# Optimization experiments

Measured on AMD Instinct MI355X. Metric: run time of the kernel, lower is better.

Reference implementation:

```python
import jax, jax.numpy as jnp
import numpy as np

# Bit-slice quantization config (MSB-first; first 1-bit slice is the sign slice)
INPUT_SLICE = (1, 2, 2, 2)    # 7 bits total
WEIGHT_SLICE = (1, 2, 2, 2)   # 7 bits total
INPUT_GRAN = 32               # input quant granularity along K (per unfolded row)
WEIGHT_GRAN_K = 32            # weight quant granularity along K
WEIGHT_GRAN_N = 32            # weight quant granularity along N
STRIDE = 1
PAD = 1
KSIZE = 3


def _quantize(x, max_abs, total_bits):
    """Symmetric per-granule quantization to signed total_bits integers."""
    max_val = float((1 << (total_bits - 1)) - 1)
    scale = max_abs / max_val
    scale = jnp.where(scale == 0, jnp.ones_like(scale), scale)
    q = jnp.clip(jnp.round(x / scale), -max_val, max_val)
    return q, scale


def _slice_recombine(q, slice_bits):
    """Emulate the bit-slice path: decompose signed int q (two's complement)
    into slices per slice_bits (MSB first), then recombine exactly as the
    crossbar MapReduce accumulation 'sum_i slice_i * 2^offset_i' would."""
    t = int(sum(slice_bits))
    qi = q.astype(jnp.int32)
    u = jnp.where(qi < 0, qi + (1 << t), qi)  # two's complement unsigned rep
    recomb = jnp.zeros_like(u)
    off = t
    for b in slice_bits:  # fixed, small slice loop
        off -= b
        s = (u >> off) & ((1 << b) - 1)
        recomb = recomb + (s << off)
    recomb = jnp.where(recomb >= (1 << (t - 1)), recomb - (1 << t), recomb)
    return recomb.astype(jnp.float32)


def _fake_quant_input(x):
    # x: (B, L, K) unfolded activations; granularity (1, INPUT_GRAN)
    B, L, K = x.shape
    g = INPUT_GRAN
    xg = x.reshape(B, L, K // g, g)
    max_abs = jnp.max(jnp.abs(xg), axis=-1, keepdims=True)
    q, scale = _quantize(xg, max_abs, sum(INPUT_SLICE))
    q = _slice_recombine(q, INPUT_SLICE)
    deq = (q * scale).reshape(B, L, K)
    # straight-through estimator (matches custom autograd conv2d_mem_func)
    return x + jax.lax.stop_gradient(deq - x)


def _fake_quant_weight(w):
    # w: (K, N) reshaped weight; granularity (WEIGHT_GRAN_K, WEIGHT_GRAN_N)
    K, N = w.shape
    gk, gn = WEIGHT_GRAN_K, WEIGHT_GRAN_N
    wg = w.reshape(K // gk, gk, N // gn, gn)
    max_abs = jnp.max(jnp.abs(wg), axis=(1, 3), keepdims=True)
    q, scale = _quantize(wg, max_abs, sum(WEIGHT_SLICE))
    q = _slice_recombine(q, WEIGHT_SLICE)
    deq = (q * scale).reshape(K, N)
    return w + jax.lax.stop_gradient(deq - w)


def _unfold(x, k, stride, pad):
    # torch.F.unfold semantics -> (B, L, C*k*k), C-major ordering
    B, C, H, W = x.shape
    xp = jnp.pad(x, ((0, 0), (0, 0), (pad, pad), (pad, pad)))
    Ho = (H + 2 * pad - k) // stride + 1
    Wo = (W + 2 * pad - k) // stride + 1
    cols = []
    for ki in range(k):  # fixed small kernel loop
        for kj in range(k):
            cols.append(xp[:, :, ki:ki + stride * Ho:stride, kj:kj + stride * Wo:stride])
    patches = jnp.stack(cols, axis=2)              # (B, C, k*k, Ho, Wo)
    patches = patches.reshape(B, C * k * k, Ho * Wo)
    return patches.transpose(0, 2, 1), Ho, Wo      # (B, L, K)


def setup_inputs() -> dict:
    key = jax.random.key(0)
    k1, k2, k3 = jax.random.split(key, 3)
    B, C, H, W = 8, 256, 56, 56
    N = 256
    fan_in = C * KSIZE * KSIZE
    x = jax.random.normal(k1, (B, C, H, W), dtype=jnp.float32)
    weight = jax.random.normal(k2, (N, C, KSIZE, KSIZE), dtype=jnp.float32) / np.sqrt(fan_in)
    bias = jax.random.normal(k3, (N,), dtype=jnp.float32) / np.sqrt(fan_in)
    return {"input": x, "weight": weight, "bias": bias}


def reference(input, weight, bias):
    B = input.shape[0]
    N = weight.shape[0]
    cols, Ho, Wo = _unfold(input, KSIZE, STRIDE, PAD)     # (B, L, K)
    w2d = weight.reshape(N, -1).T                         # (K, N)
    xq = _fake_quant_input(cols)
    wq = _fake_quant_weight(w2d)
    out = jnp.einsum('blk,kn->bln', xq, wq) + bias        # (B, L, N)
    out = out.transpose(0, 2, 1).reshape(B, N, Ho, Wo)    # fold with 1x1 kernel
    return out
```

## Files before the change

### kernel.cpp

```cpp
#include <hip/hip_runtime.h>
#include <hip/hip_bf16.h>
#include <stdint.h>

#define KD 2304
#define LD 3136
#define ND 256
#define MD 25088
#define CD 256
#define PITCH 64
#define PROWS 58
#define PLANE (PROWS * PITCH)

typedef __bf16 bf16x8 __attribute__((ext_vector_type(8)));
typedef float f32x4 __attribute__((ext_vector_type(4)));
typedef float f32x4u __attribute__((ext_vector_type(4), aligned(4)));

__device__ __forceinline__ void gload_lds16(const void* g, void* l) {
  __builtin_amdgcn_global_load_lds(
      (const __attribute__((address_space(1))) unsigned int*)g,
      (__attribute__((address_space(3))) unsigned int*)l, 16, 0, 0);
}

__global__ __launch_bounds__(256) void pad_kernel(
    const float* __restrict__ x, float* __restrict__ xpad) {
  const int plane = blockIdx.x;
  const float* src = x + (size_t)plane * LD;
  float* dst = xpad + (size_t)plane * PLANE;
  const int cc4 = (threadIdx.x & 15) * 4;
  const int r0 = threadIdx.x >> 4;
#pragma unroll
  for (int p = 0; p < 4; ++p) {
    const int r = r0 + p * 16;
    if (r >= PROWS) continue;
    f32x4 o = {0.f, 0.f, 0.f, 0.f};
    if (r >= 1 && r <= 56) {
      const float* srow = src + (r - 1) * 56;
      if (cc4 == 0) {
        f32x4u v = *(const f32x4u*)(srow);
        o[1] = v[0]; o[2] = v[1]; o[3] = v[2];
      } else if (cc4 <= 52) {
        o = *(const f32x4u*)(srow + cc4 - 1);
      } else if (cc4 == 56) {
        f32x4u v = *(const f32x4u*)(srow + 52);
        o[0] = v[3];
      }
    }
    *(f32x4*)(dst + r * PITCH + cc4) = o;
  }
}

__global__ __launch_bounds__(256) void quant_w_kernel(
    const float* __restrict__ w, __hip_bfloat16* __restrict__ wqT) {
  const int gk = blockIdx.x % 72;
  const int gn = blockIdx.x / 72;
  const int n = gn * 32 + (threadIdx.x >> 3);
  const int k = gk * 32 + (threadIdx.x & 7) * 4;
  const float4 v = *(const float4*)(w + (size_t)n * KD + k);
  float a = fmaxf(fmaxf(fabsf(v.x), fabsf(v.y)), fmaxf(fabsf(v.z), fabsf(v.w)));
#pragma unroll
  for (int m = 1; m <= 32; m <<= 1) a = fmaxf(a, __shfl_xor(a, m, 64));
  __shared__ float red[4];
  if ((threadIdx.x & 63) == 0) red[threadIdx.x >> 6] = a;
  __syncthreads();
  const float mx = fmaxf(fmaxf(red[0], red[1]), fmaxf(red[2], red[3]));
  const float r63 = (mx == 0.f) ? 0.f : 63.f / mx;
  const float scale = mx * (1.f / 63.f);
  ushort4 o;
  o.x = __builtin_bit_cast(unsigned short, __float2bfloat16(rintf(v.x * r63) * scale));
  o.y = __builtin_bit_cast(unsigned short, __float2bfloat16(rintf(v.y * r63) * scale));
  o.z = __builtin_bit_cast(unsigned short, __float2bfloat16(rintf(v.z * r63) * scale));
  o.w = __builtin_bit_cast(unsigned short, __float2bfloat16(rintf(v.w * r63) * scale));
  *(ushort4*)((unsigned short*)wqT + (size_t)n * KD + k) = o;
}

template <int KP0>
__device__ __forceinline__ void qload(const float* __restrict__ pb, int p0, int c0,
                                      f32x4u (&win)[5][3]) {
  constexpr int NCH = (KP0 + 31) / 9 + 1;
#pragma unroll
  for (int dc = 0; dc < 5; ++dc) {
    if (dc >= NCH) continue;
    const int tlo = (dc == 0) ? KP0 : 0;
    const int thi = (dc == NCH - 1) ? (KP0 + 31 - 9 * (NCH - 1)) : 8;
#pragma unroll
    for (int di = 0; di < 3; ++di) {
      if (di >= tlo / 3 && di <= thi / 3)
        win[dc][di] = *(const f32x4u*)(pb + p0 + (c0 + dc) * PLANE + di * PITCH);
    }
  }
}

template <int KP0>
__device__ __forceinline__ void qfinish(const f32x4u (&win)[5][3],
                                        char* as_row, unsigned cbase, unsigned swz) {
  float v[32];
#pragma unroll
  for (int t = 0; t < 32; ++t) {
    const int idx = KP0 + t;
    v[t] = win[idx / 9][(idx % 9) / 3][(idx % 9) % 3];
  }
  float m16[16];
#pragma unroll
  for (int t = 0; t < 16; ++t)
    m16[t] = fmaxf(__builtin_fabsf(v[2 * t]), __builtin_fabsf(v[2 * t + 1]));
#pragma unroll
  for (int t = 0; t < 8; ++t) m16[t] = fmaxf(m16[t], m16[t + 8]);
#pragma unroll
  for (int t = 0; t < 4; ++t) m16[t] = fmaxf(m16[t], m16[t + 4]);
  const float mx = fmaxf(fmaxf(m16[0], m16[1]), fmaxf(m16[2], m16[3]));
  float r63 = 63.f * __builtin_amdgcn_rcpf(mx);
  r63 = (mx == 0.f) ? 0.f : r63;
  const float scale = mx * (1.f / 63.f);
  unsigned pk[16];
#pragma unroll
  for (int t = 0; t < 16; ++t) {
    const float a = rintf(v[2 * t] * r63) * scale;
    const float b = rintf(v[2 * t + 1] * r63) * scale;
    unsigned d;
    asm("v_cvt_pk_bf16_f32 %0, %1, %2" : "=v"(d) : "v"(a), "v"(b));
    pk[t] = d;
  }
#pragma unroll
  for (int s = 0; s < 4; ++s) {
    uint4 o = {pk[4 * s], pk[4 * s + 1], pk[4 * s + 2], pk[4 * s + 3]};
    *(uint4*)(as_row + ((cbase + (unsigned)(s * 16)) ^ swz)) = o;
  }
}

__device__ __forceinline__ void stage_ns(const unsigned short* __restrict__ wsrc,
                                         int k0, int lane, int w, char* Ns) {
#pragma unroll
  for (int sg = 0; sg < 16; ++sg) {
    const int c = w * 16 + sg;
    const int rowN = c * 4 + (lane >> 4);
    const int u = (lane & 15) ^ (rowN & 7);
    gload_lds16(wsrc + (size_t)rowN * KD + k0 + u * 8,
                Ns + c * 1024 + lane * 16);
  }
}

__device__ __forceinline__ void mfma_phase(const char* As, const char* Ns,
                                           f32x4 (&acc)[4][4], int w, int lq, int hv) {
  const unsigned swq = (unsigned)((lq & 7) << 4);
#pragma unroll
  for (int kk = 0; kk < 4; ++kk) {
    const unsigned ko = (unsigned)(kk * 64 + hv * 16);
    bf16x8 af[4], bfr[4];
#pragma unroll
    for (int ifr = 0; ifr < 4; ++ifr) {
      const unsigned rn = (unsigned)(w * 64 + ifr * 16 + lq);
      af[ifr] = *(const bf16x8*)(Ns + rn * 256u + (ko ^ swq));
    }
#pragma unroll
    for (int jfr = 0; jfr < 4; ++jfr) {
      const unsigned rm = (unsigned)(jfr * 16 + lq);
      bfr[jfr] = *(const bf16x8*)(As + rm * 256u + (ko ^ swq));
    }
#pragma unroll
    for (int ifr = 0; ifr < 4; ++ifr)
#pragma unroll
      for (int jfr = 0; jfr < 4; ++jfr)
        acc[ifr][jfr] = __builtin_amdgcn_mfma_f32_16x16x32_bf16(
            af[ifr], bfr[jfr], acc[ifr][jfr], 0, 0, 0);
  }
}

#define PH(RR, W) ((128 * (RR) + 32 * (W)) % 9)

__global__ __launch_bounds__(256, 2) void fused_gemm_kernel(
    const float* __restrict__ xpad, const __hip_bfloat16* __restrict__ wqT,
    const float* __restrict__ bias, float* __restrict__ out) {
  extern __shared__ char smem[];
  char* As = smem;
  char* Ns = smem + 16384;
  const int tid = threadIdx.x;
  const int lane = tid & 63;
  const int w = __builtin_amdgcn_readfirstlane(tid >> 6);

  const int bid = blockIdx.x;
  const int mt = (bid & 7) * 49 + (bid >> 3);
  const int m0 = mt * 64;

  const int b = m0 / LD;
  const int l = m0 - b * LD + lane;
  const int i = l / 56;
  const int j = l - i * 56;
  const float* pb = xpad + (size_t)b * CD * PLANE;
  const int p0 = i * PITCH + j;
  char* as_row = As + lane * 256;
  const unsigned swz = (unsigned)((lane & 7) << 4);
  const unsigned short* wqTu = (const unsigned short*)wqT;

  const int lq = lane & 15, hv = lane >> 4;

  f32x4 acc[4][4] = {};
  f32x4u win[5][3];

#define QLOADX(RS, Rg)                                                        \
  {                                                                           \
    const int c0_ = (128 * (Rg) + 32 * w) / 9;                                \
    switch (w) {                                                              \
      case 0:  qload<PH(RS, 0)>(pb, p0, c0_, win); break;                     \
      case 1:  qload<PH(RS, 1)>(pb, p0, c0_, win); break;                     \
      case 2:  qload<PH(RS, 2)>(pb, p0, c0_, win); break;                     \
      default: qload<PH(RS, 3)>(pb, p0, c0_, win); break;                     \
    }                                                                         \
  }

#define QFINX(RS)                                                             \
  switch (w) {                                                                \
    case 0:  qfinish<PH(RS, 0)>(win, as_row, 0u,   swz); break;               \
    case 1:  qfinish<PH(RS, 1)>(win, as_row, 64u,  swz); break;               \
    case 2:  qfinish<PH(RS, 2)>(win, as_row, 128u, swz); break;               \
    default: qfinish<PH(RS, 3)>(win, as_row, 192u, swz); break;               \
  }

#define STEP(r)                                                               \
  {                                                                           \
    const int Rg = ss9 + (r);                                                 \
    stage_ns(wqTu, Rg * 128, lane, w, Ns);          \
    QFINX(r);                                          \
    if ((r) < 8 || ss == 0) { QLOADX((r) + 1, Rg + 1); }   \
    __syncthreads();                                                          \
    mfma_phase(As, Ns, acc, w, lq, hv);                                       \
    __syncthreads();                                                          \
  }

  QLOADX(0, 0);

  for (int ss = 0; ss < 2; ++ss) {
    const int ss9 = ss * 9;
    STEP(0) STEP(1) STEP(2) STEP(3) STEP(4) STEP(5) STEP(6) STEP(7) STEP(8)
  }
#undef STEP
#undef QFINX
#undef QLOADX

#pragma unroll
  for (int ifr = 0; ifr < 4; ++ifr) {
    const int nb = w * 64 + ifr * 16 + hv * 4;
    const float4 b4 = *(const float4*)&bias[nb];
#pragma unroll
    for (int jfr = 0; jfr < 4; ++jfr) {
      const int m = m0 + jfr * 16 + lq;
      const int ll = m - b * LD;
      float* op = out + ((size_t)b * ND + nb) * LD + ll;
      op[0]      = acc[ifr][jfr].x + b4.x;
      op[LD]     = acc[ifr][jfr].y + b4.y;
      op[2 * LD] = acc[ifr][jfr].z + b4.z;
      op[3 * LD] = acc[ifr][jfr].w + b4.w;
    }
  }
}

extern "C" void kernel_launch(void* const* d_in, const int* in_sizes, int n_in,
                              void* d_out, int out_size, void* d_ws, size_t ws_size,
                              hipStream_t stream) {
  const float* x = (const float*)d_in[0];
  const float* wgt = (const float*)d_in[1];
  const float* bias = (const float*)d_in[2];
  float* out = (float*)d_out;

  float* xpad = (float*)d_ws;
  __hip_bfloat16* wqT = (__hip_bfloat16*)((char*)d_ws + 30408704);

  pad_kernel<<<8 * CD, 256, 0, stream>>>(x, xpad);
  quant_w_kernel<<<576, 256, 0, stream>>>(wgt, wqT);
  fused_gemm_kernel<<<392, 256, 80 * 1024, stream>>>(xpad, wqT, bias, out);
}
```

Baseline: 79.64 us.

## Replace unrolled phase-specialized steps with rolled loop and partial-wait barriers

Replaces the fully unrolled 18-step macro schedule, which had per-wave template specializations, with a rolled loop. Each iteration dispatches qfinish on a runtime phase and always loads a fixed 5x3 window of activations, clamping the channel index. The __syncthreads calls become inline s_waitcnt vmcnt(15)/lgkmcnt(0) plus s_barrier with sched_barriers, so next-step global loads can stay in flight across the MFMA phase. This shrinks code size and instruction-cache pressure, at the cost of extra redundant loads, a runtime switch, and reliance on a hand-counted vmcnt value for correctness.

```diff
diff --git a/kernel.cpp b/kernel.cpp
--- a/kernel.cpp
+++ b/kernel.cpp
@@ -73,20 +73,15 @@
   *(ushort4*)((unsigned short*)wqT + (size_t)n * KD + k) = o;
 }
 
-template <int KP0>
-__device__ __forceinline__ void qload(const float* __restrict__ pb, int p0, int c0,
-                                      f32x4u (&win)[5][3]) {
-  constexpr int NCH = (KP0 + 31) / 9 + 1;
+__device__ __forceinline__ void qload_u(const float* __restrict__ pb, int p0,
+                                        int c0, f32x4u (&win)[5][3]) {
 #pragma unroll
   for (int dc = 0; dc < 5; ++dc) {
-    if (dc >= NCH) continue;
-    const int tlo = (dc == 0) ? KP0 : 0;
-    const int thi = (dc == NCH - 1) ? (KP0 + 31 - 9 * (NCH - 1)) : 8;
-#pragma unroll
-    for (int di = 0; di < 3; ++di) {
-      if (di >= tlo / 3 && di <= thi / 3)
-        win[dc][di] = *(const f32x4u*)(pb + p0 + (c0 + dc) * PLANE + di * PITCH);
-    }
+    const int cdc = (c0 + dc > 255) ? 255 : c0 + dc;
+    const float* cp = pb + p0 + cdc * PLANE;
+#pragma unroll
+    for (int di = 0; di < 3; ++di)
+      win[dc][di] = *(const f32x4u*)(cp + di * PITCH);
   }
 }
 
@@ -164,8 +159,6 @@
             af[ifr], bfr[jfr], acc[ifr][jfr], 0, 0, 0);
   }
 }
-
-#define PH(RR, W) ((128 * (RR) + 32 * (W)) % 9)
 
 __global__ __launch_bounds__(256, 2) void fused_gemm_kernel(
     const float* __restrict__ xpad, const __hip_bfloat16* __restrict__ wqT,
@@ -189,6 +182,7 @@
   const int p0 = i * PITCH + j;
   char* as_row = As + lane * 256;
   const unsigned swz = (unsigned)((lane & 7) << 4);
+  const unsigned cbase = (unsigned)(w * 64);
   const unsigned short* wqTu = (const unsigned short*)wqT;
 
   const int lq = lane & 15, hv = lane >> 4;
@@ -196,45 +190,37 @@
   f32x4 acc[4][4] = {};
   f32x4u win[5][3];
 
-#define QLOADX(RS, Rg)                                                        \
-  {                                                                           \
-    const int c0_ = (128 * (Rg) + 32 * w) / 9;                                \
-    switch (w) {                                                              \
-      case 0:  qload<PH(RS, 0)>(pb, p0, c0_, win); break;                     \
-      case 1:  qload<PH(RS, 1)>(pb, p0, c0_, win); break;                     \
-      case 2:  qload<PH(RS, 2)>(pb, p0, c0_, win); break;                     \
-      default: qload<PH(RS, 3)>(pb, p0, c0_, win); break;                     \
-    }                                                                         \
-  }
-
-#define QFINX(RS)                                                             \
-  switch (w) {                                                                \
-    case 0:  qfinish<PH(RS, 0)>(win, as_row, 0u,   swz); break;               \
-    case 1:  qfinish<PH(RS, 1)>(win, as_row, 64u,  swz); break;               \
-    case 2:  qfinish<PH(RS, 2)>(win, as_row, 128u, swz); break;               \
-    default: qfinish<PH(RS, 3)>(win, as_row, 192u, swz); break;               \
-  }
-
-#define STEP(r)                                                               \
-  {                                                                           \
-    const int Rg = ss9 + (r);                                                 \
-    stage_ns(wqTu, Rg * 128, lane, w, Ns);          \
-    QFINX(r);                                          \
-    if ((r) < 8 || ss == 0) { QLOADX((r) + 1, Rg + 1); }   \
-    __syncthreads();                                                          \
-    mfma_phase(As, Ns, acc, w, lq, hv);                                       \
-    __syncthreads();                                                          \
-  }
-
-  QLOADX(0, 0);
-
-  for (int ss = 0; ss < 2; ++ss) {
-    const int ss9 = ss * 9;
-    STEP(0) STEP(1) STEP(2) STEP(3) STEP(4) STEP(5) STEP(6) STEP(7) STEP(8)
-  }
-#undef STEP
-#undef QFINX
-#undef QLOADX
+  int kbase = 32 * w;
+  int ph = (32 * w) % 9;
+  qload_u(pb, p0, kbase / 9, win);
+
+  for (int R = 0; R < 18; ++R) {
+    stage_ns(wqTu, R * 128, lane, w, Ns);
+
+    switch (ph) {
+      case 0: qfinish<0>(win, as_row, cbase, swz); break;
+      case 1: qfinish<1>(win, as_row, cbase, swz); break;
+      case 2: qfinish<2>(win, as_row, cbase, swz); break;
+      case 3: qfinish<3>(win, as_row, cbase, swz); break;
+      case 4: qfinish<4>(win, as_row, cbase, swz); break;
+      case 5: qfinish<5>(win, as_row, cbase, swz); break;
+      case 6: qfinish<6>(win, as_row, cbase, swz); break;
+      default: qfinish<7>(win, as_row, cbase, swz); break;
+      case 8: qfinish<8>(win, as_row, cbase, swz); break;
+    }
+
+    kbase += 128;
+    ph += 2; if (ph >= 9) ph -= 9;
+    qload_u(pb, p0, kbase / 9, win);
+
+    asm volatile("s_waitcnt vmcnt(15) lgkmcnt(0)\n\ts_barrier" ::: "memory");
+    __builtin_amdgcn_sched_barrier(0);
+
+    mfma_phase(As, Ns, acc, w, lq, hv);
+
+    asm volatile("s_waitcnt lgkmcnt(0)\n\ts_barrier" ::: "memory");
+    __builtin_amdgcn_sched_barrier(0);
+  }
 
 #pragma unroll
   for (int ifr = 0; ifr < 4; ++ifr) {
```

Result: faster. 77.66 us (-2.5%).
